# Optimization experiments

Measured on AMD Instinct MI355X. Metric: run time of the kernel, lower is better.

The kernel has to match this reference:

```python
import jax, jax.numpy as jnp
import numpy as np
from jax import lax

B, T, U, V = 4, 256, 64, 1024   # batch, enc frames, max target len, vocab (blank=0)
F, H, HD, J = 80, 512, 512, 512  # feat dim, enc dim, dec dim, joint dim
NEG = -1e30


def setup_inputs() -> dict:
    key = jax.random.key(0)
    ks = jax.random.split(key, 10)
    inputs = jax.random.normal(ks[0], (B, T, F), dtype=jnp.float32)
    targets = jax.random.randint(ks[1], (B, U), 1, V, dtype=jnp.int32)  # labels exclude blank=0
    input_lengths = jax.random.randint(ks[2], (B,), T // 2, T + 1, dtype=jnp.int32)
    target_lengths = jax.random.randint(ks[3], (B,), U // 2, U + 1, dtype=jnp.int32)
    s = 0.02
    W_enc = jax.random.normal(ks[4], (F, H), dtype=jnp.float32) * s
    emb = jax.random.normal(ks[5], (V, HD), dtype=jnp.float32) * s
    W_jenc = jax.random.normal(ks[6], (H, J), dtype=jnp.float32) * s
    W_jdec = jax.random.normal(ks[7], (HD, J), dtype=jnp.float32) * s
    b_j = jnp.zeros((J,), dtype=jnp.float32)
    W_out = jax.random.normal(ks[8], (J, V), dtype=jnp.float32) * s
    b_out = jnp.zeros((V,), dtype=jnp.float32)
    return {"inputs": inputs, "W_enc": W_enc, "emb": emb, "W_jenc": W_jenc,
            "W_jdec": W_jdec, "b_j": b_j, "W_out": W_out, "b_out": b_out,
            "targets": targets, "input_lengths": input_lengths,
            "target_lengths": target_lengths}


def rnnt_loss(log_probs, targets, in_lens, tgt_lens):
    """RNN-T loss (blank=0, 'gather' variant: gather blank/label lps, then DP).
    log_probs: (B,T,U+1,V) log-softmaxed joint. Returns mean loss over batch."""
    Bq, Tq, U1, _ = log_probs.shape
    Uq = U1 - 1
    blank_lp = log_probs[..., 0]                                    # (B,T,U+1)
    lbl_lp = jnp.take_along_axis(
        log_probs[:, :, :Uq, :],
        jnp.broadcast_to(targets[:, None, :, None], (Bq, Tq, Uq, 1)),
        axis=3)[..., 0]                                             # (B,T,U)
    u_idx = jnp.arange(Uq)
    lbl_lp = jnp.where(u_idx[None, None, :] < tgt_lens[:, None, None], lbl_lp, NEG)

    def row(a, py):
        # a: (B,U+1) = alpha_prev + blank emission; py: (B,U) label lps this frame
        def step(c, x):
            a_u, py_prev = x
            c = jnp.logaddexp(a_u, c + py_prev)
            return c, c
        c0 = a[:, 0]
        _, rest = lax.scan(step, c0, (a[:, 1:].T, py.T))            # (U,B)
        return jnp.concatenate([c0[:, None], rest.T], axis=1)      # (B,U+1)

    # t=0 row: alpha[0,u] = cumsum of label lps at frame 0
    alpha0 = jnp.concatenate(
        [jnp.zeros((Bq, 1), log_probs.dtype),
         jnp.cumsum(lbl_lp[:, 0, :], axis=1)], axis=1)              # (B,U+1)

    def tstep(alpha_prev, x):
        blank_prev, py_t = x
        alpha = row(alpha_prev + blank_prev, py_t)
        return alpha, alpha

    xs = (jnp.swapaxes(blank_lp[:, :-1, :], 0, 1),                  # (T-1,B,U+1)
          jnp.swapaxes(lbl_lp[:, 1:, :], 0, 1))                    # (T-1,B,U)
    _, rest = lax.scan(tstep, alpha0, xs)
    alphas = jnp.concatenate([alpha0[None], rest], axis=0)          # (T,B,U+1)

    b = jnp.arange(Bq)
    t_last = in_lens - 1
    a_fin = alphas[t_last, b, tgt_lens] + blank_lp[b, t_last, tgt_lens]
    return -jnp.mean(a_fin)


def reference(inputs, W_enc, emb, W_jenc, W_jdec, b_j, W_out, b_out,
              targets, input_lengths, target_lengths):
    enc = inputs @ W_enc                                            # (B,T,H) encoder
    padded = jnp.concatenate(
        [jnp.zeros((targets.shape[0], 1), targets.dtype), targets], axis=1)
    dec = emb[padded]                                               # (B,U+1,HD) decoder
    e = enc @ W_jenc                                                # (B,T,J)
    d = dec @ W_jdec                                                # (B,U+1,J)
    h = jnp.tanh(e[:, :, None, :] + d[:, None, :, :] + b_j)        # (B,T,U+1,J)
    logits = h @ W_out + b_out                                      # (B,T,U+1,V)
    log_probs = jax.nn.log_softmax(logits, axis=-1)
    return rnnt_loss(log_probs, targets, input_lengths, target_lengths)
```

## Files before the change

kernel.cpp:

```cpp
#include <hip/hip_runtime.h>
#include <stdint.h>

#define NEGF (-1e30f)

typedef unsigned short ushort_t;
typedef unsigned char uchar_t;
typedef __attribute__((ext_vector_type(2))) long v2i64;
typedef __attribute__((ext_vector_type(4))) float f32x4;

constexpr int cB = 4, cT = 256, cU = 64, cU1 = 65, cV = 1024, cF = 80, cH = 512, cJ = 512;
constexpr int cM = cB * cT * cU1;
constexpr int cTU = cT * cU1;

__device__ __forceinline__ float tanh_fast(float x){
  float t = x * x;
  float num = x * (27.f + t);
  float den = fmaf(9.f, t, 27.f);
  float r = num * __builtin_amdgcn_rcpf(den);
  return fminf(1.f, fmaxf(-1.f, r));
}

__device__ __forceinline__ float logadd(float x, float y){
  float m = fmaxf(x, y);
  return m + __logf(1.f + __expf(-fabsf(x - y)));
}

__device__ __forceinline__ int pk8(float a, float b, float c, float d){
  int v = __builtin_amdgcn_cvt_pk_fp8_f32(a, b, 0, false);
  v = __builtin_amdgcn_cvt_pk_fp8_f32(c, d, v, true);
  return v;
}

__global__ __launch_bounds__(256) void k_pre(
    const float* __restrict__ inputs,
    const float* __restrict__ W_enc, const float* __restrict__ W_jenc,
    const float* __restrict__ emb, const int* __restrict__ targets,
    const float* __restrict__ W_jdec, const float* __restrict__ b_j,
    float* __restrict__ dmatb, float* __restrict__ e,
    const float* __restrict__ W_out, uchar_t* __restrict__ WTf8,
    float* __restrict__ S, float* __restrict__ out_loss)
{
  __shared__ float sA[4][512];
  __shared__ float sIn[4][80];
  int bid = blockIdx.x;
  int tid = threadIdx.x;

  if (bid < 256){
    int m0 = bid * 4;
    for (int i = tid; i < 320; i += 256)
      sIn[i / 80][i % 80] = inputs[m0 * 80 + i];
    __syncthreads();
    int c0 = tid, c1 = tid + 256;
    float a00 = 0.f, a01 = 0.f, a10 = 0.f, a11 = 0.f;
    float a20 = 0.f, a21 = 0.f, a30 = 0.f, a31 = 0.f;
#pragma unroll 8
    for (int k = 0; k < 80; k++){
      float w0 = W_enc[(size_t)k * 512 + c0];
      float w1 = W_enc[(size_t)k * 512 + c1];
      a00 = fmaf(sIn[0][k], w0, a00); a01 = fmaf(sIn[0][k], w1, a01);
      a10 = fmaf(sIn[1][k], w0, a10); a11 = fmaf(sIn[1][k], w1, a11);
      a20 = fmaf(sIn[2][k], w0, a20); a21 = fmaf(sIn[2][k], w1, a21);
      a30 = fmaf(sIn[3][k], w0, a30); a31 = fmaf(sIn[3][k], w1, a31);
    }
    sA[0][c0] = a00; sA[0][c1] = a01;
    sA[1][c0] = a10; sA[1][c1] = a11;
    sA[2][c0] = a20; sA[2][c1] = a21;
    sA[3][c0] = a30; sA[3][c1] = a31;
    __syncthreads();
    float b00 = 0.f, b01 = 0.f, b10 = 0.f, b11 = 0.f;
    float b20 = 0.f, b21 = 0.f, b30 = 0.f, b31 = 0.f;
#pragma unroll 8
    for (int k = 0; k < 512; k++){
      float w0 = W_jenc[(size_t)k * 512 + c0];
      float w1 = W_jenc[(size_t)k * 512 + c1];
      b00 = fmaf(sA[0][k], w0, b00); b01 = fmaf(sA[0][k], w1, b01);
      b10 = fmaf(sA[1][k], w0, b10); b11 = fmaf(sA[1][k], w1, b11);
      b20 = fmaf(sA[2][k], w0, b20); b21 = fmaf(sA[2][k], w1, b21);
      b30 = fmaf(sA[3][k], w0, b30); b31 = fmaf(sA[3][k], w1, b31);
    }
    e[(size_t)(m0 + 0) * 512 + c0] = b00; e[(size_t)(m0 + 0) * 512 + c1] = b01;
    e[(size_t)(m0 + 1) * 512 + c0] = b10; e[(size_t)(m0 + 1) * 512 + c1] = b11;
    e[(size_t)(m0 + 2) * 512 + c0] = b20; e[(size_t)(m0 + 2) * 512 + c1] = b21;
    e[(size_t)(m0 + 3) * 512 + c0] = b30; e[(size_t)(m0 + 3) * 512 + c1] = b31;
  } else if (bid < 386){
    int id = bid - 256;
    int bx = id & 1, by = id >> 1;
    int m0 = by * 4;
    int col = bx * 256 + tid;
    for (int i = tid; i < 4 * 512; i += 256){
      int r = i >> 9, c = i & 511;
      int row = m0 + r;
      int b = row / cU1, u = row % cU1;
      int src = (u == 0) ? 0 : targets[b * cU + (u - 1)];
      sA[r][c] = emb[(size_t)src * cH + c];
    }
    __syncthreads();
    float a0 = 0.f, a1 = 0.f, a2 = 0.f, a3 = 0.f;
#pragma unroll 8
    for (int k = 0; k < 512; k++){
      float bv = W_jdec[(size_t)k * cJ + col];
      a0 = fmaf(sA[0][k], bv, a0);
      a1 = fmaf(sA[1][k], bv, a1);
      a2 = fmaf(sA[2][k], bv, a2);
      a3 = fmaf(sA[3][k], bv, a3);
    }
    float bb = b_j[col];
    dmatb[(size_t)(m0 + 0) * cJ + col] = a0 + bb;
    dmatb[(size_t)(m0 + 1) * cJ + col] = a1 + bb;
    dmatb[(size_t)(m0 + 2) * cJ + col] = a2 + bb;
    dmatb[(size_t)(m0 + 3) * cJ + col] = a3 + bb;
  } else if (bid < 418){
    int id = bid - 386;
    int bn = id & 3, ksp = id >> 2;
    int lane = tid & 63, nth = tid >> 6;
    int c16 = lane & 15, quad = lane >> 4;
    int jA = ksp * 64 + quad * 8;
#pragma unroll
    for (int i = 0; i < 4; i++){
      int nt16 = nth * 4 + i;
      int n = bn * 256 + nt16 * 16 + c16;
      unsigned int p[4];
#pragma unroll
      for (int h = 0; h < 4; h++){
        int j0 = jA + (h >> 1) * 32 + (h & 1) * 4;
        float w0 = W_out[(size_t)(j0 + 0) * cV + n] * 32.f;
        float w1 = W_out[(size_t)(j0 + 1) * cV + n] * 32.f;
        float w2 = W_out[(size_t)(j0 + 2) * cV + n] * 32.f;
        float w3 = W_out[(size_t)(j0 + 3) * cV + n] * 32.f;
        p[h] = (unsigned)pk8(w0, w1, w2, w3);
      }
      uint4 pack; pack.x = p[0]; pack.y = p[1]; pack.z = p[2]; pack.w = p[3];
      *(uint4*)(WTf8 + (((size_t)(bn * 8 + ksp) * 16 + nt16) * 64 + lane) * 16) = pack;
    }
  } else {
    int i = (bid - 418) * 1024 + tid * 4;
    float4 z; z.x = 0.f; z.y = 0.f; z.z = 0.f; z.w = 0.f;
    *(float4*)(S + i) = z;
    if (bid == 418 && tid == 0) out_loss[0] = 0.f;
  }
}

__global__ __launch_bounds__(256) void k_hf(const float* __restrict__ e,
                                            const float* __restrict__ dmatb,
                                            uchar_t* __restrict__ Hbf8){
  __shared__ uchar_t sH[16 * 520];
  int tid = threadIdx.x;
  int wid = tid >> 6, lane = tid & 63;
  int c16 = lane & 15, quad = lane >> 4;
  int bm = blockIdx.x;
  int bu = bm >> 1, thalf = bm & 1;
  int b = bu / cU1;
  int t0 = thalf * 128;

  float dj[8];
  const float4* dp = (const float4*)(dmatb + (size_t)bu * cJ + lane * 8);
  float4 dA = dp[0], dB = dp[1];
  dj[0] = dA.x; dj[1] = dA.y; dj[2] = dA.z; dj[3] = dA.w;
  dj[4] = dB.x; dj[5] = dB.y; dj[6] = dB.z; dj[7] = dB.w;

  const float* erow0 = e + ((size_t)(b * cT + t0)) * cJ + lane * 8;
  uchar_t* outb = Hbf8 + (size_t)bm * 65536 + lane * 16;

  for (int mg = 0; mg < 8; mg++){
#pragma unroll
    for (int rr = 0; rr < 4; rr++){
      int rloc = wid * 4 + rr;
      const float* ep = erow0 + ((size_t)(mg * 16 + rloc)) * cJ;
      float4 e0 = *(const float4*)ep;
      float4 e1 = *(const float4*)(ep + 4);
      int v0 = pk8(tanh_fast(e0.x + dj[0]), tanh_fast(e0.y + dj[1]),
                   tanh_fast(e0.z + dj[2]), tanh_fast(e0.w + dj[3]));
      int v1 = pk8(tanh_fast(e1.x + dj[4]), tanh_fast(e1.y + dj[5]),
                   tanh_fast(e1.z + dj[6]), tanh_fast(e1.w + dj[7]));
      uint2 pk; pk.x = (unsigned)v0; pk.y = (unsigned)v1;
      *(uint2*)(sH + rloc * 520 + lane * 8) = pk;
    }
    __syncthreads();
#pragma unroll
    for (int q = 0; q < 2; q++){
      int ksp = wid * 2 + q;
      uint2 lo = *(const uint2*)(sH + c16 * 520 + ksp * 64 + quad * 8);
      uint2 hi = *(const uint2*)(sH + c16 * 520 + ksp * 64 + 32 + quad * 8);
      uint4 pack; pack.x = lo.x; pack.y = lo.y; pack.z = hi.x; pack.w = hi.y;
      *(uint4*)(outb + ((size_t)ksp * 8 + mg) * 1024) = pack;
    }
    __syncthreads();
  }
}

__global__ __launch_bounds__(256, 3) void k_joint(
    const uchar_t* __restrict__ Hbf8, const uchar_t* __restrict__ WTf8,
    const float* __restrict__ b_out, const int* __restrict__ targets,
    float* __restrict__ S,
    float* __restrict__ blank_g, float* __restrict__ lbl_g)
{
  __shared__ float redS[2][128];

  int tid = threadIdx.x;
  int wid = tid >> 6, lane = tid & 63;
  int quad = lane >> 4, c16 = lane & 15;
  int wm = wid & 1, wn = wid >> 1;
  int bid = blockIdx.x;
  int bm = ((bid >> 6) << 3) + (bid & 7);
  int bn = (bid >> 3) & 7;
  int bu = bm >> 1, thalf = bm & 1;
  int b = bu / cU1, u = bu - b * cU1;
  int tg = (u < cU) ? targets[b * cU + u] : -1;
  int lin0 = bu * cT + thalf * 128;

  f32x4 acc[4][4];
#pragma unroll
  for (int i = 0; i < 4; i++)
#pragma unroll
    for (int j = 0; j < 4; j++)
      acc[i][j] = (f32x4){0.f, 0.f, 0.f, 0.f};

  const uchar_t* aP = Hbf8 + (size_t)bm * 65536 + (wm * 4) * 1024 + lane * 16;
  const uchar_t* bP = WTf8 + (size_t)(bn >> 1) * 131072 + ((bn & 1) * 8 + wn * 4) * 1024 + lane * 16;

#pragma unroll
  for (int ksp = 0; ksp < 8; ksp++){
    v2i64 af[4], bf[4];
#pragma unroll
    for (int mt = 0; mt < 4; mt++)
      af[mt] = *(const v2i64*)(aP + (size_t)ksp * 8192 + mt * 1024);
#pragma unroll
    for (int nt = 0; nt < 4; nt++)
      bf[nt] = *(const v2i64*)(bP + (size_t)ksp * 16384 + nt * 1024);
#pragma unroll
    for (int h = 0; h < 2; h++)
#pragma unroll
      for (int mt = 0; mt < 4; mt++)
#pragma unroll
        for (int nt = 0; nt < 4; nt++)
          acc[mt][nt] = __builtin_amdgcn_mfma_f32_16x16x32_fp8_fp8(af[mt][h], bf[nt][h], acc[mt][nt], 0, 0, 0);
  }

  float bv[4];
#pragma unroll
  for (int nt = 0; nt < 4; nt++) bv[nt] = b_out[bn * 128 + (wn * 4 + nt) * 16 + c16];

  bool ownL = (tg >= 0) && ((tg >> 7) == bn) && (((tg >> 6) & 1) == wn);
  int ntO = (tg >> 4) & 3;
  int tgc = tg & 15;
  const float descale = 1.f / 32.f;

#pragma unroll
  for (int mt = 0; mt < 4; mt++){
#pragma unroll
    for (int r = 0; r < 4; r++){
      int rl = wm * 64 + mt * 16 + quad * 4 + r;
      float l[4];
#pragma unroll
      for (int nt = 0; nt < 4; nt++) l[nt] = fmaf(acc[mt][nt][r], descale, bv[nt]);
      if (bn == 0 && wn == 0 && c16 == 0) blank_g[lin0 + rl] = l[0];
      if (ownL && c16 == tgc){
        float v = l[0];
#pragma unroll
        for (int k = 1; k < 4; k++) v = (ntO == k) ? l[k] : v;
        lbl_g[lin0 + rl] = v;
      }
      float s = __expf(l[0]) + __expf(l[1]) + __expf(l[2]) + __expf(l[3]);
      s += __shfl_xor(s, 1, 64);
      s += __shfl_xor(s, 2, 64);
      s += __shfl_xor(s, 4, 64);
      s += __shfl_xor(s, 8, 64);
      if (c16 == 0) redS[wn][rl] = s;
    }
  }
  __syncthreads();
  if (tid < 128)
    atomicAdd(&S[lin0 + tid], redS[0][tid] + redS[1][tid]);
}

__global__ __launch_bounds__(256) void k_lse(
    const float* __restrict__ S, const float* __restrict__ blank_g,
    const float* __restrict__ lbl_g,
    float* __restrict__ blankd, float* __restrict__ lbld)
{
  int cell = blockIdx.x * 256 + threadIdx.x;
  float lse = __logf(S[cell]);
  int u = (cell % cTU) >> 8;
  blankd[cell] = blank_g[cell] - lse;
  lbld[cell] = (u < cU) ? (lbl_g[cell] - lse) : NEGF;
}

__global__ __launch_bounds__(256) void k_dp(
    const float* __restrict__ blankd, const float* __restrict__ lbld,
    const int* __restrict__ in_len, const int* __restrict__ tgt_len,
    float* __restrict__ out)
{
  __shared__ float sbb[cTU];
  __shared__ float slb[cTU];
  __shared__ float sS[256];
  int b = blockIdx.x;
  int tl  = tgt_len[b];
  size_t base = (size_t)b * cTU;
  for (int i = threadIdx.x; i < cTU / 4; i += 256){
    ((float4*)sbb)[i] = ((const float4*)(blankd + base))[i];
    float4 v = ((const float4*)(lbld + base))[i];
    int row = (i * 4) >> 8;
    if (row >= tl){ v.x = NEGF; v.y = NEGF; v.z = NEGF; v.w = NEGF; }
    ((float4*)slb)[i] = v;
  }
  __syncthreads();
  if (threadIdx.x >= 64) return;

  int u = threadIdx.x;
  int til = in_len[b] - 1;
  bool cap64 = (tl == 64);
  bool isTL = (u == tl);
  const float* pbu  = sbb + (u << 8);
  const float* pbu1 = sbb + (((u >= 1) ? u - 1 : 0) << 8);
  const float* plu1 = slb + (((u >= 1) ? u - 1 : 0) << 8);
  const float* plu2 = slb + (((u >= 2) ? u - 2 : 0) << 8);
  bool u1 = (u >= 1), u2 = (u >= 2);
  float fb = pbu[til];

  float A = (u == 0) ? 0.f : NEGF;
  float res = 0.f;

  auto ld = [&](const float* p, int i, bool ok) -> float {
    bool v = ok & (i >= 0) & (i <= 255);
    int ic = (i < 0) ? 0 : ((i > 255) ? 255 : i);
    float x = p[ic];
    return v ? x : NEGF;
  };

  int i0 = -u;
  float o0 = ld(pbu,  i0,     true);
  float o1 = ld(pbu,  i0 + 1, true);
  float o2 = ld(plu1, i0 + 1, u1);
  float o3 = ld(pbu1, i0 + 1, u1);
  float o4 = ld(plu1, i0 + 2, u1);
  float o5 = ld(plu2, i0 + 2, u2);

  for (int g = 0; g < 159; g++){
    float c0 = o0, c1 = o1, c2 = o2, c3 = o3, c4 = o4, c5 = o5;
    int i0n = i0 + 2;
    o0 = ld(pbu,  i0n,     true);
    o1 = ld(pbu,  i0n + 1, true);
    o2 = ld(plu1, i0n + 1, u1);
    o3 = ld(pbu1, i0n + 1, u1);
    o4 = ld(plu1, i0n + 2, u1);
    o5 = ld(plu2, i0n + 2, u2);

    float up1 = __shfl_up(A, 1, 64);
    float up2 = __shfl_up(A, 2, 64);

    float C0 = c0 + c1;
    float C1 = logadd(c2 + c1, c3 + c4);
    float C2 = c5 + c4;

    bool tv1 = (i0 + 1 >= 0) & (i0 + 1 <= 255);
    float Amid = logadd(A + c0, up1 + c2);
    Amid = tv1 ? Amid : NEGF;
    bool tv2 = (i0 + 2 >= 0) & (i0 + 2 <= 255);
    float Anew = logadd(logadd(A + C0, up1 + C1), up2 + C2);
    Anew = tv2 ? Anew : NEGF;

    if (isTL && (i0 + 1) == til) res = Amid + fb;
    if (isTL && (i0 + 2) == til) res = Anew + fb;
    if (u == 63){
      if (tv1) sS[i0 + 1] = Amid;
      if (tv2) sS[i0 + 2] = Anew;
    }
    A = Anew;
    i0 = i0n;
  }

  if (cap64){
    const float* pb64 = sbb + (64 << 8);
    const float* pl63 = slb + (63 << 8);
    float A64 = sS[0] + pl63[0];
    for (int t = 1; t <= til; t++)
      A64 = logadd(A64 + pb64[t - 1], sS[t] + pl63[t]);
    if (u == 0) res = A64 + pb64[til];
  }

  res += __shfl_xor(res, 1, 64);
  res += __shfl_xor(res, 2, 64);
  res += __shfl_xor(res, 4, 64);
  res += __shfl_xor(res, 8, 64);
  res += __shfl_xor(res, 16, 64);
  res += __shfl_xor(res, 32, 64);
  if (u == 0) atomicAdd(out, -0.25f * res);
}

extern "C" void kernel_launch(void* const* d_in, const int* in_sizes, int n_in,
                              void* d_out, int out_size, void* d_ws, size_t ws_size,
                              hipStream_t stream)
{
  (void)in_sizes; (void)n_in; (void)out_size; (void)ws_size;
  const float* inputs = (const float*)d_in[0];
  const float* W_enc  = (const float*)d_in[1];
  const float* emb    = (const float*)d_in[2];
  const float* W_jenc = (const float*)d_in[3];
  const float* W_jdec = (const float*)d_in[4];
  const float* b_j    = (const float*)d_in[5];
  const float* W_out  = (const float*)d_in[6];
  const float* b_out  = (const float*)d_in[7];
  const int* targets  = (const int*)d_in[8];
  const int* in_len   = (const int*)d_in[9];
  const int* tgt_len  = (const int*)d_in[10];

  char* w = (char*)d_ws;
  auto alloc = [&](size_t bytes){ char* p = w; w += (bytes + 255) & ~(size_t)255; return p; };
  float* e       = (float*)alloc((size_t)1024 * 512 * 4);
  float* dmatb   = (float*)alloc((size_t)260 * 512 * 4);
  float* blank_g = (float*)alloc((size_t)cM * 4);
  float* lbl_g   = (float*)alloc((size_t)cM * 4);
  float* S       = (float*)alloc((size_t)cM * 4);
  float* blankd  = (float*)alloc((size_t)cM * 4);
  float* lbld    = (float*)alloc((size_t)cM * 4);
  uchar_t* Hbf8  = (uchar_t*)alloc((size_t)520 * 65536);
  uchar_t* WTf8  = (uchar_t*)alloc((size_t)4 * 131072);

  k_pre<<<483, 256, 0, stream>>>(inputs, W_enc, W_jenc, emb, targets, W_jdec, b_j,
                                 dmatb, e, W_out, WTf8, S, (float*)d_out);
  k_hf<<<520, 256, 0, stream>>>(e, dmatb, Hbf8);
  k_joint<<<4160, 256, 0, stream>>>(Hbf8, WTf8, b_out, targets, S, blank_g, lbl_g);
  k_lse<<<260, 256, 0, stream>>>(S, blank_g, lbl_g, blankd, lbld);
  k_dp<<<4, 256, 0, stream>>>(blankd, lbld, in_len, tgt_len, (float*)d_out);
}
```

Measured before the change: 241.8 us.

## Fuse log-sum-exp normalization into DP kernel and run DP in base-2 log domain

Removes the separate k_lse kernel: the DP kernel now reads S, blank and label logits directly, applies the log normalization while filling shared memory, and skips rows beyond the target length. The whole alpha recursion is rescaled to log2 units so that raw exp2/log2 hardware intrinsics replace __expf/__logf, and the final sum is multiplied by ln2/4. The three-way logadd becomes a single max plus three exp2 terms, and the shuffles use ds_bpermute with the loop unrolled by 3. This saves one launch and two full-size intermediate buffers written and read through global memory, and shortens the serial DP chain. In exchange it adds more numeric approximation from the raw intrinsics.

```diff
diff --git a/kernel.cpp b/kernel.cpp
--- a/kernel.cpp
+++ b/kernel.cpp
@@ -20,9 +20,9 @@
   return fminf(1.f, fmaxf(-1.f, r));
 }
 
-__device__ __forceinline__ float logadd(float x, float y){
+__device__ __forceinline__ float logadd2(float x, float y){
   float m = fmaxf(x, y);
-  return m + __logf(1.f + __expf(-fabsf(x - y)));
+  return m + __builtin_amdgcn_logf(1.f + __builtin_amdgcn_exp2f(-fabsf(x - y)));
 }
 
 __device__ __forceinline__ int pk8(float a, float b, float c, float d){
@@ -273,35 +273,40 @@
     atomicAdd(&S[lin0 + tid], redS[0][tid] + redS[1][tid]);
 }
 
-__global__ __launch_bounds__(256) void k_lse(
+__global__ __launch_bounds__(256) void k_dp(
     const float* __restrict__ S, const float* __restrict__ blank_g,
     const float* __restrict__ lbl_g,
-    float* __restrict__ blankd, float* __restrict__ lbld)
-{
-  int cell = blockIdx.x * 256 + threadIdx.x;
-  float lse = __logf(S[cell]);
-  int u = (cell % cTU) >> 8;
-  blankd[cell] = blank_g[cell] - lse;
-  lbld[cell] = (u < cU) ? (lbl_g[cell] - lse) : NEGF;
-}
-
-__global__ __launch_bounds__(256) void k_dp(
-    const float* __restrict__ blankd, const float* __restrict__ lbld,
     const int* __restrict__ in_len, const int* __restrict__ tgt_len,
     float* __restrict__ out)
 {
   __shared__ float sbb[cTU];
   __shared__ float slb[cTU];
   __shared__ float sS[256];
+  constexpr float LOG2E = 1.4426950408889634f;
   int b = blockIdx.x;
   int tl  = tgt_len[b];
   size_t base = (size_t)b * cTU;
   for (int i = threadIdx.x; i < cTU / 4; i += 256){
-    ((float4*)sbb)[i] = ((const float4*)(blankd + base))[i];
-    float4 v = ((const float4*)(lbld + base))[i];
-    int row = (i * 4) >> 8;
-    if (row >= tl){ v.x = NEGF; v.y = NEGF; v.z = NEGF; v.w = NEGF; }
-    ((float4*)slb)[i] = v;
+    int row = i >> 6;
+    if (row > tl) continue;
+    float4 sv = ((const float4*)(S + base))[i];
+    float4 bvv = ((const float4*)(blank_g + base))[i];
+    float4 ls;
+    ls.x = __builtin_amdgcn_logf(sv.x); ls.y = __builtin_amdgcn_logf(sv.y);
+    ls.z = __builtin_amdgcn_logf(sv.z); ls.w = __builtin_amdgcn_logf(sv.w);
+    float4 bo;
+    bo.x = fmaf(bvv.x, LOG2E, -ls.x); bo.y = fmaf(bvv.y, LOG2E, -ls.y);
+    bo.z = fmaf(bvv.z, LOG2E, -ls.z); bo.w = fmaf(bvv.w, LOG2E, -ls.w);
+    ((float4*)sbb)[i] = bo;
+    float4 lo;
+    if (row < tl){
+      float4 lv = ((const float4*)(lbl_g + base))[i];
+      lo.x = fmaf(lv.x, LOG2E, -ls.x); lo.y = fmaf(lv.y, LOG2E, -ls.y);
+      lo.z = fmaf(lv.z, LOG2E, -ls.z); lo.w = fmaf(lv.w, LOG2E, -ls.w);
+    } else {
+      lo.x = NEGF; lo.y = NEGF; lo.z = NEGF; lo.w = NEGF;
+    }
+    ((float4*)slb)[i] = lo;
   }
   __syncthreads();
   if (threadIdx.x >= 64) return;
@@ -316,15 +321,15 @@
   const float* plu2 = slb + (((u >= 2) ? u - 2 : 0) << 8);
   bool u1 = (u >= 1), u2 = (u >= 2);
   float fb = pbu[til];
+  int shA1 = (u - 1) << 2;
+  int shA2 = (u - 2) << 2;
 
   float A = (u == 0) ? 0.f : NEGF;
   float res = 0.f;
 
   auto ld = [&](const float* p, int i, bool ok) -> float {
-    bool v = ok & (i >= 0) & (i <= 255);
-    int ic = (i < 0) ? 0 : ((i > 255) ? 255 : i);
-    float x = p[ic];
-    return v ? x : NEGF;
+    float x = p[i & 255];
+    return (ok & ((unsigned)i < 256u)) ? x : NEGF;
   };
 
   int i0 = -u;
@@ -335,28 +340,34 @@
   float o4 = ld(plu1, i0 + 2, u1);
   float o5 = ld(plu2, i0 + 2, u2);
 
+#pragma unroll 3
   for (int g = 0; g < 159; g++){
-    float c0 = o0, c1 = o1, c2 = o2, c3 = o3, c4 = o4, c5 = o5;
+    float up1 = __int_as_float(__builtin_amdgcn_ds_bpermute(shA1, __float_as_int(A)));
+    float up2 = __int_as_float(__builtin_amdgcn_ds_bpermute(shA2, __float_as_int(A)));
+
     int i0n = i0 + 2;
-    o0 = ld(pbu,  i0n,     true);
-    o1 = ld(pbu,  i0n + 1, true);
-    o2 = ld(plu1, i0n + 1, u1);
-    o3 = ld(pbu1, i0n + 1, u1);
-    o4 = ld(plu1, i0n + 2, u1);
-    o5 = ld(plu2, i0n + 2, u2);
-
-    float up1 = __shfl_up(A, 1, 64);
-    float up2 = __shfl_up(A, 2, 64);
-
-    float C0 = c0 + c1;
-    float C1 = logadd(c2 + c1, c3 + c4);
-    float C2 = c5 + c4;
-
-    bool tv1 = (i0 + 1 >= 0) & (i0 + 1 <= 255);
-    float Amid = logadd(A + c0, up1 + c2);
+    float n0 = ld(pbu,  i0n,     true);
+    float n1 = ld(pbu,  i0n + 1, true);
+    float n2 = ld(plu1, i0n + 1, u1);
+    float n3 = ld(pbu1, i0n + 1, u1);
+    float n4 = ld(plu1, i0n + 2, u1);
+    float n5 = ld(plu2, i0n + 2, u2);
+
+    float C0 = o0 + o1;
+    float C1 = logadd2(o2 + o1, o3 + o4);
+    float C2 = o5 + o4;
+
+    float am0 = A + o0, am1 = up1 + o2;
+    float Amid = logadd2(am0, am1);
+    bool tv1 = ((unsigned)(i0 + 1) < 256u);
     Amid = tv1 ? Amid : NEGF;
-    bool tv2 = (i0 + 2 >= 0) & (i0 + 2 <= 255);
-    float Anew = logadd(logadd(A + C0, up1 + C1), up2 + C2);
+
+    float a0 = A + C0, a1 = up1 + C1, a2 = up2 + C2;
+    float m3 = fmaxf(fmaxf(a0, a1), a2);
+    float s3 = __builtin_amdgcn_exp2f(a0 - m3) + __builtin_amdgcn_exp2f(a1 - m3)
+             + __builtin_amdgcn_exp2f(a2 - m3);
+    float Anew = m3 + __builtin_amdgcn_logf(s3);
+    bool tv2 = ((unsigned)(i0 + 2) < 256u);
     Anew = tv2 ? Anew : NEGF;
 
     if (isTL && (i0 + 1) == til) res = Amid + fb;
@@ -367,6 +378,7 @@
     }
     A = Anew;
     i0 = i0n;
+    o0 = n0; o1 = n1; o2 = n2; o3 = n3; o4 = n4; o5 = n5;
   }
 
   if (cap64){
@@ -374,7 +386,7 @@
     const float* pl63 = slb + (63 << 8);
     float A64 = sS[0] + pl63[0];
     for (int t = 1; t <= til; t++)
-      A64 = logadd(A64 + pb64[t - 1], sS[t] + pl63[t]);
+      A64 = logadd2(A64 + pb64[t - 1], sS[t] + pl63[t]);
     if (u == 0) res = A64 + pb64[til];
   }
 
@@ -384,7 +396,7 @@
   res += __shfl_xor(res, 8, 64);
   res += __shfl_xor(res, 16, 64);
   res += __shfl_xor(res, 32, 64);
-  if (u == 0) atomicAdd(out, -0.25f * res);
+  if (u == 0) atomicAdd(out, -0.17328679513998632f * res);
 }
 
 extern "C" void kernel_launch(void* const* d_in, const int* in_sizes, int n_in,
@@ -411,8 +423,6 @@
   float* blank_g = (float*)alloc((size_t)cM * 4);
   float* lbl_g   = (float*)alloc((size_t)cM * 4);
   float* S       = (float*)alloc((size_t)cM * 4);
-  float* blankd  = (float*)alloc((size_t)cM * 4);
-  float* lbld    = (float*)alloc((size_t)cM * 4);
   uchar_t* Hbf8  = (uchar_t*)alloc((size_t)520 * 65536);
   uchar_t* WTf8  = (uchar_t*)alloc((size_t)4 * 131072);
 
@@ -420,6 +430,5 @@
                                  dmatb, e, W_out, WTf8, S, (float*)d_out);
   k_hf<<<520, 256, 0, stream>>>(e, dmatb, Hbf8);
   k_joint<<<4160, 256, 0, stream>>>(Hbf8, WTf8, b_out, targets, S, blank_g, lbl_g);
-  k_lse<<<260, 256, 0, stream>>>(S, blank_g, lbl_g, blankd, lbld);
-  k_dp<<<4, 256, 0, stream>>>(blankd, lbld, in_len, tgt_len, (float*)d_out);
-}
+  k_dp<<<4, 256, 0, stream>>>(S, blank_g, lbl_g, in_len, tgt_len, (float*)d_out);
+}
```

Result: faster. 226.7 us (-6.3%).
